# Performance work log

Hardware: AMD Instinct MI355X
Metric: run time of the kernel (lower is better)

The kernel has to match this reference:

```python
import jax, jax.numpy as jnp
import numpy as np

B, T, D, HEADS = 2, 2048, 512, 8

def setup_inputs() -> dict:
    key = jax.random.key(0)
    k1, k2 = jax.random.split(key)
    h = jax.random.normal(k1, (B, T, D), dtype=jnp.float32)
    # xavier_uniform over (heads, d, d): fan_in = fan_out = d
    limit = float(np.sqrt(6.0 / (D + D)))
    A = jax.random.uniform(k2, (HEADS, D, D), dtype=jnp.float32, minval=-limit, maxval=limit)
    return {"h": h, "A": A}

def reference(h, A):
    Bb, Tt, d = h.shape
    heads = A.shape[0]
    # per-head bilinear scores: (h @ A_i) @ h^T  -> (B, heads, T, T)
    scores = jnp.einsum('btd,hde,bse->bhts', h, A, h)
    causal = jnp.tril(jnp.ones((Tt, Tt), dtype=bool))  # (T, T)
    scores = jnp.where(causal[None, None], scores, -jnp.inf)
    attn = jax.nn.softmax(scores, axis=-1)  # (B, heads, T, T)
    out = jnp.einsum('bhts,bsd->bhtd', attn, h)  # (B, heads, T, d)
    # torch .view(B, T, -1) on contiguous (B, heads, T, d): raw row-major reshape
    return out.reshape(Bb, Tt, heads * d)
```

## Files before the change

kernel.cpp:

```cpp
#include <hip/hip_runtime.h>

typedef unsigned short ushort_t;
typedef __attribute__((ext_vector_type(8))) short bf16x8;
typedef __attribute__((ext_vector_type(4))) float f32x4;
typedef __attribute__((ext_vector_type(4))) unsigned short u16x4;

#define T_DIM 2048
#define D_DIM 512
#define NH 8
#define NB 2
#define SLOT_F 16384
#define SLOT_U 32768

static __device__ __forceinline__ ushort_t f2bf(float x) {
  union { float f; unsigned u; } v; v.f = x;
  unsigned r = v.u + 0x7fffu + ((v.u >> 16) & 1u);
  return (ushort_t)(r >> 16);
}
static __device__ __forceinline__ float bf2f(ushort_t b) {
  union { unsigned u; float f; } v; v.u = ((unsigned)b) << 16;
  return v.f;
}
static __device__ __forceinline__ f32x4 mfma16(bf16x8 a, bf16x8 b, f32x4 c) {
  return __builtin_amdgcn_mfma_f32_16x16x32_bf16(a, b, c, 0, 0, 0);
}

typedef const __attribute__((address_space(1))) unsigned asg_t;
typedef __attribute__((address_space(3))) unsigned asl_t;
static __device__ __forceinline__ void gload16(const ushort_t* g, ushort_t* l) {
  __builtin_amdgcn_global_load_lds((asg_t*)g, (asl_t*)l, 16, 0, 0);
}

static __device__ __forceinline__ void stage128x32(const ushort_t* __restrict__ src,
                                                   size_t ldk, ushort_t* lds, int tid) {
  int w = tid >> 6;
#pragma unroll
  for (int p = 0; p < 2; ++p) {
    int t = p * 256 + tid;
    int r = t >> 2;
    int col = (t & 3) << 3;
    gload16(src + (size_t)r * ldk + col, lds + p * 2048 + (w << 9));
  }
}

static __device__ __forceinline__ void decode_bh(int j, int nbc, int& bl, int& hd) {
  if (nbc == 2) { bl = j & 1; hd = j >> 1; } else { bl = 0; hd = j; }
}

__global__ __launch_bounds__(256) void split_h_kernel(const float* __restrict__ h,
    ushort_t* __restrict__ hhi, ushort_t* __restrict__ hlo, ushort_t* __restrict__ hT) {
  __shared__ ushort_t lds[64][68];
  int x = blockIdx.x;
  int b = x >> 8, tt = (x >> 3) & 31, ee = x & 7;
  int t0 = tt * 64, e0 = ee * 64;
  int rr = threadIdx.x >> 4;
  int c4 = (threadIdx.x & 15) * 4;
#pragma unroll
  for (int it = 0; it < 4; ++it) {
    int t = it * 16 + rr;
    size_t idx = ((size_t)(b * T_DIM + t0 + t)) * D_DIM + e0 + c4;
    float4 v = *(const float4*)(h + idx);
    u16x4 hv, lv;
    hv[0] = f2bf(v.x); lv[0] = f2bf(v.x - bf2f(hv[0]));
    hv[1] = f2bf(v.y); lv[1] = f2bf(v.y - bf2f(hv[1]));
    hv[2] = f2bf(v.z); lv[2] = f2bf(v.z - bf2f(hv[2]));
    hv[3] = f2bf(v.w); lv[3] = f2bf(v.w - bf2f(hv[3]));
    *(u16x4*)(hhi + idx) = hv;
    *(u16x4*)(hlo + idx) = lv;
    *(u16x4*)&lds[t][c4] = hv;
  }
  __syncthreads();
#pragma unroll
  for (int it = 0; it < 4; ++it) {
    int e = it * 16 + rr;
    u16x4 wv;
    wv[0] = lds[c4 + 0][e];
    wv[1] = lds[c4 + 1][e];
    wv[2] = lds[c4 + 2][e];
    wv[3] = lds[c4 + 3][e];
    *(u16x4*)(hT + ((size_t)(b * D_DIM + e0 + e)) * T_DIM + t0 + c4) = wv;
  }
}

__global__ __launch_bounds__(256) void split_AT_kernel(const float* __restrict__ A,
    ushort_t* __restrict__ AThi, ushort_t* __restrict__ ATlo) {
  __shared__ ushort_t ldh[64][68];
  __shared__ ushort_t ldl[64][68];
  int x = blockIdx.x;
  int hd = x >> 6, dd = (x >> 3) & 7, ee = x & 7;
  int d0 = dd * 64, e0 = ee * 64;
  int rr = threadIdx.x >> 4;
  int c4 = (threadIdx.x & 15) * 4;
#pragma unroll
  for (int it = 0; it < 4; ++it) {
    int d = it * 16 + rr;
    float4 v = *(const float4*)(A + ((size_t)(hd * D_DIM + d0 + d)) * D_DIM + e0 + c4);
    u16x4 hv, lv;
    hv[0] = f2bf(v.x); lv[0] = f2bf(v.x - bf2f(hv[0]));
    hv[1] = f2bf(v.y); lv[1] = f2bf(v.y - bf2f(hv[1]));
    hv[2] = f2bf(v.z); lv[2] = f2bf(v.z - bf2f(hv[2]));
    hv[3] = f2bf(v.w); lv[3] = f2bf(v.w - bf2f(hv[3]));
    *(u16x4*)&ldh[d][c4] = hv;
    *(u16x4*)&ldl[d][c4] = lv;
  }
  __syncthreads();
#pragma unroll
  for (int it = 0; it < 4; ++it) {
    int e = it * 16 + rr;
    u16x4 wh, wl;
    wh[0] = ldh[c4 + 0][e]; wl[0] = ldl[c4 + 0][e];
    wh[1] = ldh[c4 + 1][e]; wl[1] = ldl[c4 + 1][e];
    wh[2] = ldh[c4 + 2][e]; wl[2] = ldl[c4 + 2][e];
    wh[3] = ldh[c4 + 3][e]; wl[3] = ldl[c4 + 3][e];
    size_t o = ((size_t)(hd * D_DIM + e0 + e)) * D_DIM + d0 + c4;
    *(u16x4*)(AThi + o) = wh;
    *(u16x4*)(ATlo + o) = wl;
  }
}

__global__ __launch_bounds__(256, 2) void qgemm_kernel(
    const ushort_t* __restrict__ hhi, const ushort_t* __restrict__ hlo,
    const ushort_t* __restrict__ AThi, const ushort_t* __restrict__ ATlo,
    ushort_t* __restrict__ Qhi, ushort_t* __restrict__ Qlo) {
  __shared__ ushort_t lAh[128 * 32], lAl[128 * 32], lBh[128 * 32], lBl[128 * 32];
  int bid = blockIdx.x;
  int hd = bid & 7;
  int rem = bid >> 3;
  int nt = rem & 3;
  int mt = (rem >> 2) & 15;
  int b = rem >> 6;
  int bh = b * NH + hd;
  int tid = threadIdx.x;
  int w = tid >> 6, lane = tid & 63;
  int g = lane >> 4, c = lane & 15;
  int m0 = (w >> 1) * 64, n0 = (w & 1) * 64;
  const ushort_t* Ah = hhi + (size_t)b * T_DIM * D_DIM + (size_t)(mt * 128) * D_DIM;
  const ushort_t* Al = hlo + (size_t)b * T_DIM * D_DIM + (size_t)(mt * 128) * D_DIM;
  const ushort_t* Bh = AThi + (size_t)hd * D_DIM * D_DIM + (size_t)(nt * 128) * D_DIM;
  const ushort_t* Bl = ATlo + (size_t)hd * D_DIM * D_DIM + (size_t)(nt * 128) * D_DIM;
  f32x4 zero4 = {0.f, 0.f, 0.f, 0.f};
  f32x4 acc[4][4];
#pragma unroll
  for (int i = 0; i < 4; ++i)
#pragma unroll
    for (int j = 0; j < 4; ++j) acc[i][j] = zero4;
  for (int kc = 0; kc < 16; ++kc) {
    int k0 = kc * 32;
    stage128x32(Ah + k0, D_DIM, lAh, tid);
    stage128x32(Al + k0, D_DIM, lAl, tid);
    stage128x32(Bh + k0, D_DIM, lBh, tid);
    stage128x32(Bl + k0, D_DIM, lBl, tid);
    __syncthreads();
    bf16x8 ah[4], al[4], bh8[4], bl8[4];
#pragma unroll
    for (int mf = 0; mf < 4; ++mf) {
      int ro = (m0 + 16 * mf + c) * 32 + g * 8;
      ah[mf] = *(const bf16x8*)&lAh[ro];
      al[mf] = *(const bf16x8*)&lAl[ro];
    }
#pragma unroll
    for (int nf = 0; nf < 4; ++nf) {
      int ro = (n0 + 16 * nf + c) * 32 + g * 8;
      bh8[nf] = *(const bf16x8*)&lBh[ro];
      bl8[nf] = *(const bf16x8*)&lBl[ro];
    }
#pragma unroll
    for (int mf = 0; mf < 4; ++mf)
#pragma unroll
      for (int nf = 0; nf < 4; ++nf) {
        acc[mf][nf] = mfma16(ah[mf], bh8[nf], acc[mf][nf]);
        acc[mf][nf] = mfma16(ah[mf], bl8[nf], acc[mf][nf]);
        acc[mf][nf] = mfma16(al[mf], bh8[nf], acc[mf][nf]);
      }
    __syncthreads();
  }
  size_t qbase = (size_t)bh * T_DIM * D_DIM;
#pragma unroll
  for (int mf = 0; mf < 4; ++mf)
#pragma unroll
    for (int nf = 0; nf < 4; ++nf)
#pragma unroll
      for (int i2 = 0; i2 < 4; ++i2) {
        int q = mt * 128 + m0 + 16 * mf + 4 * g + i2;
        int e = nt * 128 + n0 + 16 * nf + c;
        float v = acc[mf][nf][i2];
        ushort_t hi = f2bf(v);
        ushort_t lo = f2bf(v - bf2f(hi));
        Qhi[qbase + (size_t)q * D_DIM + e] = hi;
        Qlo[qbase + (size_t)q * D_DIM + e] = lo;
      }
}

__global__ __launch_bounds__(256, 2) void sgemm_kernel(
    const ushort_t* __restrict__ Qhi, const ushort_t* __restrict__ Qlo,
    const ushort_t* __restrict__ Khi, const ushort_t* __restrict__ Klo,
    float* __restrict__ S, int b0, int nbc) {
  __shared__ ushort_t lAh[128 * 32], lAl[128 * 32], lBh[128 * 32], lBl[128 * 32];
  int mlanes = nbc * 8;
  int i = blockIdx.x;
  int j = i % mlanes, ti = i / mlanes;
  int bl, hd;
  decode_bh(j, nbc, bl, hd);
  int b = b0 + bl;
  int bh = b * NH + hd;
  int bhl = bl * NH + hd;
  int tq = (int)((sqrtf(8.f * (float)ti + 1.f) - 1.f) * 0.5f);
  while ((tq + 1) * (tq + 2) / 2 <= ti) ++tq;
  while (tq * (tq + 1) / 2 > ti) --tq;
  int ts = ti - tq * (tq + 1) / 2;
  int tid = threadIdx.x;
  int w = tid >> 6, lane = tid & 63;
  int g = lane >> 4, c = lane & 15;
  int m0 = (w >> 1) * 64, n0 = (w & 1) * 64;
  const ushort_t* Ah = Qhi + (size_t)bh * T_DIM * D_DIM + (size_t)(tq * 128) * D_DIM;
  const ushort_t* Al = Qlo + (size_t)bh * T_DIM * D_DIM + (size_t)(tq * 128) * D_DIM;
  const ushort_t* Bh = Khi + (size_t)b * T_DIM * D_DIM + (size_t)(ts * 128) * D_DIM;
  const ushort_t* Bl = Klo + (size_t)b * T_DIM * D_DIM + (size_t)(ts * 128) * D_DIM;
  f32x4 zero4 = {0.f, 0.f, 0.f, 0.f};
  f32x4 acc[4][4];
#pragma unroll
  for (int ii = 0; ii < 4; ++ii)
#pragma unroll
    for (int jj = 0; jj < 4; ++jj) acc[ii][jj] = zero4;
  for (int kc = 0; kc < 16; ++kc) {
    int k0 = kc * 32;
    stage128x32(Ah + k0, D_DIM, lAh, tid);
    stage128x32(Al + k0, D_DIM, lAl, tid);
    stage128x32(Bh + k0, D_DIM, lBh, tid);
    stage128x32(Bl + k0, D_DIM, lBl, tid);
    __syncthreads();
    bf16x8 ah[4], al[4], bh8[4], bl8[4];
#pragma unroll
    for (int mf = 0; mf < 4; ++mf) {
      int ro = (m0 + 16 * mf + c) * 32 + g * 8;
      ah[mf] = *(const bf16x8*)&lAh[ro];
      al[mf] = *(const bf16x8*)&lAl[ro];
    }
#pragma unroll
    for (int nf = 0; nf < 4; ++nf) {
      int ro = (n0 + 16 * nf + c) * 32 + g * 8;
      bh8[nf] = *(const bf16x8*)&lBh[ro];
      bl8[nf] = *(const bf16x8*)&lBl[ro];
    }
#pragma unroll
    for (int mf = 0; mf < 4; ++mf)
#pragma unroll
      for (int nf = 0; nf < 4; ++nf) {
        acc[mf][nf] = mfma16(ah[mf], bh8[nf], acc[mf][nf]);
        acc[mf][nf] = mfma16(ah[mf], bl8[nf], acc[mf][nf]);
        acc[mf][nf] = mfma16(al[mf], bh8[nf], acc[mf][nf]);
      }
    __syncthreads();
  }
  float* Sslot = S + ((size_t)(bhl * 136 + tq * (tq + 1) / 2 + ts)) * SLOT_F;
#pragma unroll
  for (int mf = 0; mf < 4; ++mf)
#pragma unroll
    for (int nf = 0; nf < 4; ++nf)
#pragma unroll
      for (int i2 = 0; i2 < 4; ++i2) {
        int lq = m0 + 16 * mf + 4 * g + i2;
        int ls = n0 + 16 * nf + c;
        Sslot[(size_t)lq * 128 + ls] = acc[mf][nf][i2];
      }
}

__global__ __launch_bounds__(256) void softmax_kernel(float* __restrict__ S, int nbc) {
  __shared__ float rowbuf[2048];
  __shared__ float red[4];
  int mlanes = nbc * 8;
  int i = blockIdx.x;
  int j = i % mlanes, q = i / mlanes;
  int bl, hd;
  decode_bh(j, nbc, bl, hd);
  int bhl = bl * NH + hd;
  int tq = q >> 7, lq = q & 127;
  float* Sb = S + (size_t)bhl * 136 * SLOT_F;
  size_t rowf = (size_t)(tq * (tq + 1) / 2) * SLOT_F + (size_t)lq * 128;
  int n = q + 1;
  int nout = (tq + 1) << 7;
  int tid = threadIdx.x;
  float mx = -3.0e38f;
  for (int s0 = tid * 4; s0 < nout; s0 += 1024) {
    int ts = s0 >> 7;
    const float* src = Sb + rowf + (size_t)ts * SLOT_F + (s0 & 127);
    float4 v = make_float4(-3.0e38f, -3.0e38f, -3.0e38f, -3.0e38f);
    if (s0 < n) v = *(const float4*)src;
    float a0 = (s0 + 0 < n) ? v.x : -3.0e38f;
    float a1 = (s0 + 1 < n) ? v.y : -3.0e38f;
    float a2 = (s0 + 2 < n) ? v.z : -3.0e38f;
    float a3 = (s0 + 3 < n) ? v.w : -3.0e38f;
    rowbuf[s0 + 0] = a0; rowbuf[s0 + 1] = a1;
    rowbuf[s0 + 2] = a2; rowbuf[s0 + 3] = a3;
    mx = fmaxf(mx, fmaxf(fmaxf(a0, a1), fmaxf(a2, a3)));
  }
#pragma unroll
  for (int off = 1; off < 64; off <<= 1) mx = fmaxf(mx, __shfl_xor(mx, off));
  if ((tid & 63) == 0) red[tid >> 6] = mx;
  __syncthreads();
  mx = fmaxf(fmaxf(red[0], red[1]), fmaxf(red[2], red[3]));
  float sum = 0.f;
  for (int s0 = tid * 4; s0 < nout; s0 += 1024) {
    float e0 = __expf(rowbuf[s0 + 0] - mx);
    float e1 = __expf(rowbuf[s0 + 1] - mx);
    float e2 = __expf(rowbuf[s0 + 2] - mx);
    float e3 = __expf(rowbuf[s0 + 3] - mx);
    rowbuf[s0 + 0] = e0; rowbuf[s0 + 1] = e1;
    rowbuf[s0 + 2] = e2; rowbuf[s0 + 3] = e3;
    sum += (e0 + e1) + (e2 + e3);
  }
#pragma unroll
  for (int off = 1; off < 64; off <<= 1) sum += __shfl_xor(sum, off);
  __syncthreads();
  if ((tid & 63) == 0) red[tid >> 6] = sum;
  __syncthreads();
  float inv = 1.0f / ((red[0] + red[1]) + (red[2] + red[3]));
  for (int s0 = tid * 4; s0 < nout; s0 += 1024) {
    int ts = s0 >> 7;
    ushort_t* dst = (ushort_t*)Sb + 2 * (rowf + (size_t)ts * SLOT_F) + (s0 & 127);
    u16x4 o;
    o[0] = f2bf(rowbuf[s0 + 0] * inv);
    o[1] = f2bf(rowbuf[s0 + 1] * inv);
    o[2] = f2bf(rowbuf[s0 + 2] * inv);
    o[3] = f2bf(rowbuf[s0 + 3] * inv);
    *(u16x4*)dst = o;
  }
}

__global__ __launch_bounds__(256, 2) void pv_kernel(const ushort_t* __restrict__ P,
    const ushort_t* __restrict__ hT, float* __restrict__ out, int b0, int nbc) {
  __shared__ ushort_t lA[128 * 32], lB[128 * 32];
  int mlanes = nbc * 8;
  int i = blockIdx.x;
  int j = i % mlanes;
  int rem = i / mlanes;
  int nt = rem & 3;
  int tq = 15 - (rem >> 2);
  int bl, hd;
  decode_bh(j, nbc, bl, hd);
  int b = b0 + bl;
  int bhl = bl * NH + hd;
  int tid = threadIdx.x;
  int w = tid >> 6, lane = tid & 63;
  int g = lane >> 4, c = lane & 15;
  int m0 = (w >> 1) * 64, n0 = (w & 1) * 64;
  size_t pslot = (size_t)(bhl * 136 + tq * (tq + 1) / 2);
  const ushort_t* Bb = hT + (size_t)b * D_DIM * T_DIM + (size_t)(nt * 128) * T_DIM;
  f32x4 zero4 = {0.f, 0.f, 0.f, 0.f};
  f32x4 acc[4][4];
#pragma unroll
  for (int ii = 0; ii < 4; ++ii)
#pragma unroll
    for (int jj = 0; jj < 4; ++jj) acc[ii][jj] = zero4;
  int nk = (tq + 1) * 4;
  for (int kc = 0; kc < nk; ++kc) {
    const ushort_t* Asrc = P + (pslot + (kc >> 2)) * SLOT_U + ((kc & 3) << 5);
    stage128x32(Asrc, 256, lA, tid);
    stage128x32(Bb + kc * 32, T_DIM, lB, tid);
    __syncthreads();
    bf16x8 af[4], bf[4];
#pragma unroll
    for (int mf = 0; mf < 4; ++mf)
      af[mf] = *(const bf16x8*)&lA[(m0 + 16 * mf + c) * 32 + g * 8];
#pragma unroll
    for (int nf = 0; nf < 4; ++nf)
      bf[nf] = *(const bf16x8*)&lB[(n0 + 16 * nf + c) * 32 + g * 8];
#pragma unroll
    for (int mf = 0; mf < 4; ++mf)
#pragma unroll
      for (int nf = 0; nf < 4; ++nf) acc[mf][nf] = mfma16(af[mf], bf[nf], acc[mf][nf]);
    __syncthreads();
  }
  size_t obase = (size_t)((b * NH + hd)) * T_DIM * D_DIM;
#pragma unroll
  for (int mf = 0; mf < 4; ++mf)
#pragma unroll
    for (int nf = 0; nf < 4; ++nf)
#pragma unroll
      for (int i2 = 0; i2 < 4; ++i2) {
        int q = tq * 128 + m0 + 16 * mf + 4 * g + i2;
        int d = nt * 128 + n0 + 16 * nf + c;
        out[obase + (size_t)q * D_DIM + d] = acc[mf][nf][i2];
      }
}

extern "C" void kernel_launch(void* const* d_in, const int* in_sizes, int n_in,
                              void* d_out, int out_size, void* d_ws, size_t ws_size,
                              hipStream_t stream) {
  const float* h = (const float*)d_in[0];
  const float* A = (const float*)d_in[1];
  float* out = (float*)d_out;
  char* ws = (char*)d_ws;
  const size_t SZ_H = (size_t)NB * T_DIM * D_DIM * sizeof(ushort_t);
  const size_t SZ_A = (size_t)NH * D_DIM * D_DIM * sizeof(ushort_t);
  const size_t SZ_Q = (size_t)NB * NH * T_DIM * D_DIM * sizeof(ushort_t);
  const size_t SZ_SB = 136ull * SLOT_F * sizeof(float) * NH;
  const size_t FIXED = 3 * SZ_H + 2 * SZ_A + 2 * SZ_Q;
  ushort_t* hhi  = (ushort_t*)(ws);
  ushort_t* hlo  = (ushort_t*)(ws + SZ_H);
  ushort_t* hT   = (ushort_t*)(ws + 2 * SZ_H);
  ushort_t* AThi = (ushort_t*)(ws + 3 * SZ_H);
  ushort_t* ATlo = (ushort_t*)(ws + 3 * SZ_H + SZ_A);
  ushort_t* Qhi  = (ushort_t*)(ws + 3 * SZ_H + 2 * SZ_A);
  ushort_t* Qlo  = (ushort_t*)(ws + 3 * SZ_H + 2 * SZ_A + SZ_Q);
  float*    Sbuf = (float*)   (ws + FIXED);

  int nbc = (FIXED + 2 * SZ_SB <= ws_size) ? 2 : 1;

  split_h_kernel<<<512, 256, 0, stream>>>(h, hhi, hlo, hT);
  split_AT_kernel<<<512, 256, 0, stream>>>(A, AThi, ATlo);
  qgemm_kernel<<<1024, 256, 0, stream>>>(hhi, hlo, AThi, ATlo, Qhi, Qlo);
  for (int b0 = 0; b0 < NB; b0 += nbc) {
    sgemm_kernel<<<nbc * 8 * 136, 256, 0, stream>>>(Qhi, Qlo, hhi, hlo, Sbuf, b0, nbc);
    softmax_kernel<<<nbc * 8 * 2048, 256, 0, stream>>>(Sbuf, nbc);
    pv_kernel<<<nbc * 512, 256, 0, stream>>>((const ushort_t*)Sbuf, hT, out, b0, nbc);
  }
}
```

Measured before the change: 354.3 us.

## Fuse softmax stats into score GEMM and apply normalization inside PV

New measurement: 430.1 us. +21.4%, slower.

```diff
diff --git a/kernel.cpp b/kernel.cpp
--- a/kernel.cpp
+++ b/kernel.cpp
@@ -10,7 +10,6 @@
 #define NH 8
 #define NB 2
 #define SLOT_F 16384
-#define SLOT_U 32768
 
 static __device__ __forceinline__ ushort_t f2bf(float x) {
   union { float f; unsigned u; } v; v.f = x;
@@ -194,7 +193,8 @@
 __global__ __launch_bounds__(256, 2) void sgemm_kernel(
     const ushort_t* __restrict__ Qhi, const ushort_t* __restrict__ Qlo,
     const ushort_t* __restrict__ Khi, const ushort_t* __restrict__ Klo,
-    float* __restrict__ S, int b0, int nbc) {
+    float* __restrict__ S, float* __restrict__ statm, float* __restrict__ statl,
+    int b0, int nbc) {
   __shared__ ushort_t lAh[128 * 32], lAl[128 * 32], lBh[128 * 32], lBl[128 * 32];
   int mlanes = nbc * 8;
   int i = blockIdx.x;
@@ -252,7 +252,8 @@
       }
     __syncthreads();
   }
-  float* Sslot = S + ((size_t)(bhl * 136 + tq * (tq + 1) / 2 + ts)) * SLOT_F;
+  size_t slot = (size_t)(bhl * 136 + tq * (tq + 1) / 2 + ts);
+  float* Sslot = S + slot * SLOT_F;
 #pragma unroll
   for (int mf = 0; mf < 4; ++mf)
 #pragma unroll
@@ -263,73 +264,94 @@
         int ls = n0 + 16 * nf + c;
         Sslot[(size_t)lq * 128 + ls] = acc[mf][nf][i2];
       }
-}
-
-__global__ __launch_bounds__(256) void softmax_kernel(float* __restrict__ S, int nbc) {
-  __shared__ float rowbuf[2048];
-  __shared__ float red[4];
+  float* smax = (float*)lAh;
+  float* ssum = (float*)lAl;
+  float* mfin = (float*)lBh;
+  int diag = (ts == tq);
+  float rm[16];
+#pragma unroll
+  for (int mf = 0; mf < 4; ++mf)
+#pragma unroll
+    for (int i2 = 0; i2 < 4; ++i2) {
+      int idx = mf * 4 + i2;
+      int row_l = m0 + 16 * mf + 4 * g + i2;
+      float v = -3.0e38f;
+#pragma unroll
+      for (int nf = 0; nf < 4; ++nf) {
+        int col_l = n0 + 16 * nf + c;
+        if (!diag || col_l <= row_l) v = fmaxf(v, acc[mf][nf][i2]);
+      }
+      rm[idx] = v;
+    }
+#pragma unroll
+  for (int off = 1; off < 16; off <<= 1)
+#pragma unroll
+    for (int idx = 0; idx < 16; ++idx) rm[idx] = fmaxf(rm[idx], __shfl_xor(rm[idx], off));
+  if (c == 0) {
+#pragma unroll
+    for (int mf = 0; mf < 4; ++mf)
+#pragma unroll
+      for (int i2 = 0; i2 < 4; ++i2)
+        smax[(w & 1) * 128 + m0 + 16 * mf + 4 * g + i2] = rm[mf * 4 + i2];
+  }
+  __syncthreads();
+  if (tid < 128) mfin[tid] = fmaxf(smax[tid], smax[128 + tid]);
+  __syncthreads();
+  float rs[16];
+#pragma unroll
+  for (int mf = 0; mf < 4; ++mf)
+#pragma unroll
+    for (int i2 = 0; i2 < 4; ++i2) {
+      int idx = mf * 4 + i2;
+      int row_l = m0 + 16 * mf + 4 * g + i2;
+      float mrow = mfin[row_l];
+      float s_ = 0.f;
+#pragma unroll
+      for (int nf = 0; nf < 4; ++nf) {
+        int col_l = n0 + 16 * nf + c;
+        if (!diag || col_l <= row_l) s_ += __expf(acc[mf][nf][i2] - mrow);
+      }
+      rs[idx] = s_;
+    }
+#pragma unroll
+  for (int off = 1; off < 16; off <<= 1)
+#pragma unroll
+    for (int idx = 0; idx < 16; ++idx) rs[idx] += __shfl_xor(rs[idx], off);
+  if (c == 0) {
+#pragma unroll
+    for (int mf = 0; mf < 4; ++mf)
+#pragma unroll
+      for (int i2 = 0; i2 < 4; ++i2)
+        ssum[(w & 1) * 128 + m0 + 16 * mf + 4 * g + i2] = rs[mf * 4 + i2];
+  }
+  __syncthreads();
+  if (tid < 128) {
+    statm[slot * 128 + tid] = mfin[tid];
+    statl[slot * 128 + tid] = ssum[tid] + ssum[128 + tid];
+  }
+}
+
+__global__ __launch_bounds__(128) void combine_kernel(const float* __restrict__ statm,
+    const float* __restrict__ statl, float2* __restrict__ mst, int nbc) {
   int mlanes = nbc * 8;
-  int i = blockIdx.x;
-  int j = i % mlanes, q = i / mlanes;
-  int bl, hd;
-  decode_bh(j, nbc, bl, hd);
-  int bhl = bl * NH + hd;
-  int tq = q >> 7, lq = q & 127;
-  float* Sb = S + (size_t)bhl * 136 * SLOT_F;
-  size_t rowf = (size_t)(tq * (tq + 1) / 2) * SLOT_F + (size_t)lq * 128;
-  int n = q + 1;
-  int nout = (tq + 1) << 7;
-  int tid = threadIdx.x;
-  float mx = -3.0e38f;
-  for (int s0 = tid * 4; s0 < nout; s0 += 1024) {
-    int ts = s0 >> 7;
-    const float* src = Sb + rowf + (size_t)ts * SLOT_F + (s0 & 127);
-    float4 v = make_float4(-3.0e38f, -3.0e38f, -3.0e38f, -3.0e38f);
-    if (s0 < n) v = *(const float4*)src;
-    float a0 = (s0 + 0 < n) ? v.x : -3.0e38f;
-    float a1 = (s0 + 1 < n) ? v.y : -3.0e38f;
-    float a2 = (s0 + 2 < n) ? v.z : -3.0e38f;
-    float a3 = (s0 + 3 < n) ? v.w : -3.0e38f;
-    rowbuf[s0 + 0] = a0; rowbuf[s0 + 1] = a1;
-    rowbuf[s0 + 2] = a2; rowbuf[s0 + 3] = a3;
-    mx = fmaxf(mx, fmaxf(fmaxf(a0, a1), fmaxf(a2, a3)));
-  }
-#pragma unroll
-  for (int off = 1; off < 64; off <<= 1) mx = fmaxf(mx, __shfl_xor(mx, off));
-  if ((tid & 63) == 0) red[tid >> 6] = mx;
-  __syncthreads();
-  mx = fmaxf(fmaxf(red[0], red[1]), fmaxf(red[2], red[3]));
-  float sum = 0.f;
-  for (int s0 = tid * 4; s0 < nout; s0 += 1024) {
-    float e0 = __expf(rowbuf[s0 + 0] - mx);
-    float e1 = __expf(rowbuf[s0 + 1] - mx);
-    float e2 = __expf(rowbuf[s0 + 2] - mx);
-    float e3 = __expf(rowbuf[s0 + 3] - mx);
-    rowbuf[s0 + 0] = e0; rowbuf[s0 + 1] = e1;
-    rowbuf[s0 + 2] = e2; rowbuf[s0 + 3] = e3;
-    sum += (e0 + e1) + (e2 + e3);
-  }
-#pragma unroll
-  for (int off = 1; off < 64; off <<= 1) sum += __shfl_xor(sum, off);
-  __syncthreads();
-  if ((tid & 63) == 0) red[tid >> 6] = sum;
-  __syncthreads();
-  float inv = 1.0f / ((red[0] + red[1]) + (red[2] + red[3]));
-  for (int s0 = tid * 4; s0 < nout; s0 += 1024) {
-    int ts = s0 >> 7;
-    ushort_t* dst = (ushort_t*)Sb + 2 * (rowf + (size_t)ts * SLOT_F) + (s0 & 127);
-    u16x4 o;
-    o[0] = f2bf(rowbuf[s0 + 0] * inv);
-    o[1] = f2bf(rowbuf[s0 + 1] * inv);
-    o[2] = f2bf(rowbuf[s0 + 2] * inv);
-    o[3] = f2bf(rowbuf[s0 + 3] * inv);
-    *(u16x4*)dst = o;
-  }
-}
-
-__global__ __launch_bounds__(256, 2) void pv_kernel(const ushort_t* __restrict__ P,
-    const ushort_t* __restrict__ hT, float* __restrict__ out, int b0, int nbc) {
+  int bid = blockIdx.x;
+  int bhl = bid % mlanes;
+  int tq = bid / mlanes;
+  int r = threadIdx.x;
+  size_t base = (size_t)(bhl * 136 + tq * (tq + 1) / 2);
+  float m = -3.0e38f;
+  for (int t = 0; t <= tq; ++t) m = fmaxf(m, statm[(base + t) * 128 + r]);
+  float l = 0.f;
+  for (int t = 0; t <= tq; ++t)
+    l += __expf(statm[(base + t) * 128 + r] - m) * statl[(base + t) * 128 + r];
+  mst[((size_t)(bhl * 16 + tq)) * 128 + r] = make_float2(m, 1.0f / l);
+}
+
+__global__ __launch_bounds__(256, 2) void pv_kernel(const float* __restrict__ Sf,
+    const float2* __restrict__ mst, const ushort_t* __restrict__ hT,
+    float* __restrict__ out, int b0, int nbc) {
   __shared__ ushort_t lA[128 * 32], lB[128 * 32];
+  __shared__ float2 ml[128];
   int mlanes = nbc * 8;
   int i = blockIdx.x;
   int j = i % mlanes;
@@ -346,6 +368,8 @@
   int m0 = (w >> 1) * 64, n0 = (w & 1) * 64;
   size_t pslot = (size_t)(bhl * 136 + tq * (tq + 1) / 2);
   const ushort_t* Bb = hT + (size_t)b * D_DIM * T_DIM + (size_t)(nt * 128) * T_DIM;
+  for (int r = tid; r < 128; r += 256) ml[r] = mst[((size_t)(bhl * 16 + tq)) * 128 + r];
+  __syncthreads();
   f32x4 zero4 = {0.f, 0.f, 0.f, 0.f};
   f32x4 acc[4][4];
 #pragma unroll
@@ -354,8 +378,28 @@
     for (int jj = 0; jj < 4; ++jj) acc[ii][jj] = zero4;
   int nk = (tq + 1) * 4;
   for (int kc = 0; kc < nk; ++kc) {
-    const ushort_t* Asrc = P + (pslot + (kc >> 2)) * SLOT_U + ((kc & 3) << 5);
-    stage128x32(Asrc, 256, lA, tid);
+    int ti_ = kc >> 2;
+    int diag = (ti_ == tq);
+    int w0 = (kc & 3) << 5;
+    const float* Af = Sf + (pslot + ti_) * SLOT_F + w0;
+#pragma unroll
+    for (int p = 0; p < 2; ++p) {
+      int tt = p * 256 + tid;
+      int r = tt >> 2, cb = (tt & 3) << 3;
+      const float* src = Af + (size_t)r * 128 + cb;
+      float4 v0 = *(const float4*)src;
+      float4 v1 = *(const float4*)(src + 4);
+      float2 s_ = ml[r];
+      int lim = diag ? (r - w0 - cb) : 7;
+      float e[8] = {v0.x, v0.y, v0.z, v0.w, v1.x, v1.y, v1.z, v1.w};
+      union { bf16x8 v8; ushort_t u[8]; } pk;
+#pragma unroll
+      for (int jj = 0; jj < 8; ++jj) {
+        float ev = __expf(e[jj] - s_.x) * s_.y;
+        pk.u[jj] = (jj <= lim) ? f2bf(ev) : (ushort_t)0;
+      }
+      *(bf16x8*)&lA[r * 32 + cb] = pk.v8;
+    }
     stage128x32(Bb + kc * 32, T_DIM, lB, tid);
     __syncthreads();
     bf16x8 af[4], bf[4];
@@ -405,14 +449,25 @@
   ushort_t* Qlo  = (ushort_t*)(ws + 3 * SZ_H + 2 * SZ_A + SZ_Q);
   float*    Sbuf = (float*)   (ws + FIXED);
 
-  int nbc = (FIXED + 2 * SZ_SB <= ws_size) ? 2 : 1;
+  int nbc = 2;
+  for (;;) {
+    size_t stat1 = (size_t)nbc * 8 * 136 * 128 * sizeof(float);
+    size_t mstsz = (size_t)nbc * 8 * 16 * 128 * sizeof(float2);
+    if (FIXED + (size_t)nbc * SZ_SB + 2 * stat1 + mstsz <= ws_size || nbc == 1) break;
+    nbc = 1;
+  }
+  size_t stat1 = (size_t)nbc * 8 * 136 * 128 * sizeof(float);
+  float*  statm = (float*)(ws + FIXED + (size_t)nbc * SZ_SB);
+  float*  statl = (float*)(ws + FIXED + (size_t)nbc * SZ_SB + stat1);
+  float2* mst   = (float2*)(ws + FIXED + (size_t)nbc * SZ_SB + 2 * stat1);
 
   split_h_kernel<<<512, 256, 0, stream>>>(h, hhi, hlo, hT);
   split_AT_kernel<<<512, 256, 0, stream>>>(A, AThi, ATlo);
   qgemm_kernel<<<1024, 256, 0, stream>>>(hhi, hlo, AThi, ATlo, Qhi, Qlo);
   for (int b0 = 0; b0 < NB; b0 += nbc) {
-    sgemm_kernel<<<nbc * 8 * 136, 256, 0, stream>>>(Qhi, Qlo, hhi, hlo, Sbuf, b0, nbc);
-    softmax_kernel<<<nbc * 8 * 2048, 256, 0, stream>>>(Sbuf, nbc);
-    pv_kernel<<<nbc * 512, 256, 0, stream>>>((const ushort_t*)Sbuf, hT, out, b0, nbc);
-  }
-}
+    sgemm_kernel<<<nbc * 8 * 136, 256, 0, stream>>>(Qhi, Qlo, hhi, hlo, Sbuf,
+                                                    statm, statl, b0, nbc);
+    combine_kernel<<<nbc * 8 * 16, 128, 0, stream>>>(statm, statl, mst, nbc);
+    pv_kernel<<<nbc * 512, 256, 0, stream>>>(Sbuf, mst, hT, out, b0, nbc);
+  }
+}
```
